# Performance work log

Measured on AMD Instinct MI355X. Metric: run time of the kernel, lower is better.

## Reference

```python
import jax, jax.numpy as jnp
import numpy as np

KERNEL_PARA = 1.0

def setup_inputs() -> dict:
    key = jax.random.key(0)
    k1, k2 = jax.random.split(key)
    H1 = jax.random.normal(k1, (8192, 64), dtype=jnp.float32)
    H2 = jax.random.normal(k2, (8192, 64), dtype=jnp.float32)
    return {"H1": H1, "H2": H2}

def reference(H1, H2):
    # S[ij] = exp(-delta * ||x_i - x_j||^2), via ||a||^2 + ||b||^2 - 2 a.b
    H11 = jnp.sum(H1 * H1, axis=1)[:, None]          # [n1, 1]
    H22 = jnp.sum(H2 * H2, axis=1)[None, :]          # [1, n2]
    H12 = jnp.matmul(H1, H2.T)                        # [n1, n2]
    D_2 = H11 + H22 - 2.0 * H12
    return jnp.exp(-KERNEL_PARA * D_2)
```

## Files before the change

kernel.cpp:

```cpp
#include <hip/hip_runtime.h>
#include <hip/hip_bf16.h>


typedef float  f32x4  __attribute__((ext_vector_type(4)));
typedef short  short8 __attribute__((ext_vector_type(8)));
typedef unsigned short ushort8 __attribute__((ext_vector_type(8)));

#define KD 64
#define TM 128
#define TN 128

__device__ __forceinline__ unsigned short f2bf(float x) {
    __hip_bfloat16 h = __float2bfloat16(x);
    unsigned short u;
    __builtin_memcpy(&u, &h, 2);
    return u;
}
__device__ __forceinline__ float bf2f(unsigned short u) {
    unsigned int v = ((unsigned int)u) << 16;
    float f;
    __builtin_memcpy(&f, &v, 4);
    return f;
}

__device__ __forceinline__ unsigned panel_off(unsigned row, unsigned kcByte) {
    return (row * 128u + kcByte) ^ ((row & 7u) << 4);
}

__global__ __launch_bounds__(512, 4) void gauss_mfma(
    const float* __restrict__ H1, const float* __restrict__ H2,
    float* __restrict__ out, int N2)
{
    __shared__ __align__(16) unsigned char sAhi[TM * KD * 2];
    __shared__ __align__(16) unsigned char sAlo[TM * KD * 2];
    __shared__ __align__(16) unsigned char sBhi[TN * KD * 2];
    __shared__ __align__(16) unsigned char sBlo[TN * KD * 2];
    __shared__ __align__(16) float snrm[TM + TN];

    const int t    = threadIdx.x;
    const int lane = t & 63, w = t >> 6;
    const int wr = w >> 2, wc = w & 3;
    const int lr = lane & 15;
    const int kb = lane >> 4;
    const int r4 = kb * 4;
    const int row0 = blockIdx.y * TM;
    const int col0 = blockIdx.x * TN;

    #pragma unroll
    for (int side = 0; side < 2; ++side) {
        const float* src = side ? (H2 + (size_t)col0 * KD)
                                : (H1 + (size_t)row0 * KD);
        unsigned char* hi = side ? sBhi : sAhi;
        unsigned char* lo = side ? sBlo : sAlo;
        #pragma unroll
        for (int i = 0; i < 2; ++i) {
            int g   = i * 512 + t;
            int row = g >> 3;
            int kc  = g & 7;
            const f32x4* p = (const f32x4*)(src + (size_t)g * 8);
            f32x4 v0 = p[0], v1 = p[1];
            ushort8 h, l;
            float s = 0.f;
            #pragma unroll
            for (int e = 0; e < 8; ++e) {
                float a = (e < 4) ? v0[e] : v1[e - 4];
                unsigned short hb = f2bf(a);
                h[e] = hb;
                l[e] = f2bf(a - bf2f(hb));
                s = fmaf(a, a, s);
            }
            s += __shfl_xor(s, 1);
            s += __shfl_xor(s, 2);
            s += __shfl_xor(s, 4);
            unsigned off = panel_off((unsigned)row, (unsigned)kc * 16u);
            *(ushort8*)(hi + off) = h;
            *(ushort8*)(lo + off) = l;
            if (kc == 0) snrm[side * TM + row] = s;
        }
    }
    __syncthreads();

    float n1v[4];
    f32x4 n2v[2];
    #pragma unroll
    for (int fr = 0; fr < 4; ++fr)
        n1v[fr] = snrm[wr * 64 + fr * 16 + lr];
    #pragma unroll
    for (int fc = 0; fc < 2; ++fc)
        n2v[fc] = *(const f32x4*)&snrm[TM + wc * 32 + fc * 16 + r4];

    f32x4 acc[4][2];
    #pragma unroll
    for (int a = 0; a < 4; ++a)
        #pragma unroll
        for (int b = 0; b < 2; ++b)
            acc[a][b] = (f32x4){0.f, 0.f, 0.f, 0.f};

    #pragma unroll
    for (int ks = 0; ks < 2; ++ks) {
        const unsigned kByte = (unsigned)(ks * 64 + kb * 16);
        short8 ah[4], al[4];
        #pragma unroll
        for (int fr = 0; fr < 4; ++fr) {
            const unsigned off = panel_off((unsigned)(wr * 64 + fr * 16 + lr), kByte);
            ah[fr] = *(const short8*)(sAhi + off);
            al[fr] = *(const short8*)(sAlo + off);
        }
        #pragma unroll
        for (int fc = 0; fc < 2; ++fc) {
            const unsigned off = panel_off((unsigned)(wc * 32 + fc * 16 + lr), kByte);
            short8 bh = *(const short8*)(sBhi + off);
            short8 bl = *(const short8*)(sBlo + off);
            #pragma unroll
            for (int fr = 0; fr < 4; ++fr) {
                acc[fr][fc] = __builtin_amdgcn_mfma_f32_16x16x32_bf16(bh, ah[fr], acc[fr][fc], 0, 0, 0);
                acc[fr][fc] = __builtin_amdgcn_mfma_f32_16x16x32_bf16(bl, ah[fr], acc[fr][fc], 0, 0, 0);
                acc[fr][fc] = __builtin_amdgcn_mfma_f32_16x16x32_bf16(bh, al[fr], acc[fr][fc], 0, 0, 0);
            }
        }
    }

    #pragma unroll
    for (int fr = 0; fr < 4; ++fr) {
        const int grow = row0 + wr * 64 + fr * 16 + lr;
        float* orow = out + (size_t)grow * (size_t)N2 + (col0 + wc * 32 + r4);
        #pragma unroll
        for (int fc = 0; fc < 2; ++fc) {
            f32x4 cst;
            #pragma unroll
            for (int j = 0; j < 4; ++j) {
                float d2 = fmaf(-2.0f, acc[fr][fc][j], n1v[fr] + n2v[fc][j]);
                cst[j] = __expf(-d2);
            }
            *(f32x4*)(orow + fc * 16) = cst;
        }
    }
}

extern "C" void kernel_launch(void* const* d_in, const int* in_sizes, int n_in,
                              void* d_out, int out_size, void* d_ws, size_t ws_size,
                              hipStream_t stream) {
    const float* H1 = (const float*)d_in[0];
    const float* H2 = (const float*)d_in[1];
    float* out = (float*)d_out;
    const int n1 = in_sizes[0] / KD;
    const int n2 = in_sizes[1] / KD;
    dim3 grid(n2 / TN, n1 / TM);
    gauss_mfma<<<grid, dim3(512), 0, stream>>>(H1, H2, out, n2);
}
```

Before: 61.90 us.

## Precompute bf16 hi/lo splits and norms in prep kernel, load fragments from global

Adds a prep kernel that splits H1 and H2 into bf16 hi/lo planes and row norms once, storing them in workspace. The main kernel then skips the per-tile conversion and the LDS staging, reading MFMA fragments straight from global memory. It uses 256-thread blocks with 4 waves, each owning a 64x64 subtile. This removes conversion work that was repeated across every tile, at the cost of an extra launch, uncoalesced-ish global fragment loads, and more accumulator registers. A fallback to the old kernel remains for when the workspace is too small.

Measured after the change: 106.8 us. 72.5% more time.

```diff
diff --git a/kernel.cpp b/kernel.cpp
--- a/kernel.cpp
+++ b/kernel.cpp
@@ -7,8 +7,11 @@
 typedef unsigned short ushort8 __attribute__((ext_vector_type(8)));
 
 #define KD 64
-#define TM 128
-#define TN 128
+
+#define PLANE  (1u << 20)
+#define OFF_N1 (4u * PLANE)
+#define OFF_N2 (4u * PLANE + 8192u * 4u)
+#define WS_NEED ((size_t)(4u * PLANE + 2u * 8192u * 4u))
 
 __device__ __forceinline__ unsigned short f2bf(float x) {
     __hip_bfloat16 h = __float2bfloat16(x);
@@ -23,40 +26,146 @@
     return f;
 }
 
+__global__ __launch_bounds__(256) void gauss_prep(const float* __restrict__ H1,
+                                                  const float* __restrict__ H2,
+                                                  unsigned char* __restrict__ ws)
+{
+    const int cid   = blockIdx.x * 256 + threadIdx.x;
+    const int which = cid >> 16;
+    const int g     = cid & 65535;
+    const int row   = g >> 3;
+    const int kc    = g & 7;
+
+    const float* src = which ? H2 : H1;
+    const f32x4* p = (const f32x4*)(src + (size_t)g * 8);
+    f32x4 v0 = p[0], v1 = p[1];
+
+    ushort8 h, l;
+    float s = 0.f;
+    #pragma unroll
+    for (int e = 0; e < 8; ++e) {
+        float a = (e < 4) ? v0[e] : v1[e - 4];
+        unsigned short hb = f2bf(a);
+        h[e] = hb;
+        l[e] = f2bf(a - bf2f(hb));
+        s = fmaf(a, a, s);
+    }
+    s += __shfl_xor(s, 1);
+    s += __shfl_xor(s, 2);
+    s += __shfl_xor(s, 4);
+
+    unsigned char* hi = ws + (which ? 2u * PLANE : 0u) + (size_t)g * 16u;
+    unsigned char* lo = hi + PLANE;
+    *(ushort8*)hi = h;
+    *(ushort8*)lo = l;
+    if (kc == 0)
+        *(float*)(ws + (which ? OFF_N2 : OFF_N1) + (size_t)row * 4u) = s;
+}
+
+__global__ __launch_bounds__(256, 3) void gauss_main(
+    const unsigned char* __restrict__ ws, float* __restrict__ out, int N2)
+{
+    const int t    = threadIdx.x;
+    const int lane = t & 63, w = t >> 6;
+    const int wr = w >> 1, wc = w & 1;
+    const int lr = lane & 15;
+    const int kb = lane >> 4;
+    const int r4 = kb * 4;
+    const int row0 = blockIdx.y * 128;
+    const int col0 = blockIdx.x * 128;
+
+    const unsigned char* hi1 = ws;
+    const unsigned char* lo1 = ws + PLANE;
+    const unsigned char* hi2 = ws + 2u * PLANE;
+    const unsigned char* lo2 = ws + 3u * PLANE;
+    const float* nrm1 = (const float*)(ws + OFF_N1);
+    const float* nrm2 = (const float*)(ws + OFF_N2);
+
+    float n1v[4];
+    f32x4 n2v[4];
+    #pragma unroll
+    for (int fr = 0; fr < 4; ++fr)
+        n1v[fr] = nrm1[row0 + wr * 64 + fr * 16 + lr];
+    #pragma unroll
+    for (int fc = 0; fc < 4; ++fc)
+        n2v[fc] = *(const f32x4*)(nrm2 + col0 + wc * 64 + fc * 16 + r4);
+
+    f32x4 acc[4][4];
+    #pragma unroll
+    for (int a = 0; a < 4; ++a)
+        #pragma unroll
+        for (int b = 0; b < 4; ++b)
+            acc[a][b] = (f32x4){0.f, 0.f, 0.f, 0.f};
+
+    #pragma unroll
+    for (int ks = 0; ks < 2; ++ks) {
+        const unsigned kByte = (unsigned)(ks * 64 + kb * 16);
+        short8 ah[4], al[4];
+        #pragma unroll
+        for (int fr = 0; fr < 4; ++fr) {
+            size_t off = (size_t)(row0 + wr * 64 + fr * 16 + lr) * 128u + kByte;
+            ah[fr] = *(const short8*)(hi1 + off);
+            al[fr] = *(const short8*)(lo1 + off);
+        }
+        #pragma unroll
+        for (int fc = 0; fc < 4; ++fc) {
+            size_t off = (size_t)(col0 + wc * 64 + fc * 16 + lr) * 128u + kByte;
+            short8 bh = *(const short8*)(hi2 + off);
+            short8 bl = *(const short8*)(lo2 + off);
+            #pragma unroll
+            for (int fr = 0; fr < 4; ++fr) {
+                acc[fr][fc] = __builtin_amdgcn_mfma_f32_16x16x32_bf16(bh, ah[fr], acc[fr][fc], 0, 0, 0);
+                acc[fr][fc] = __builtin_amdgcn_mfma_f32_16x16x32_bf16(bl, ah[fr], acc[fr][fc], 0, 0, 0);
+                acc[fr][fc] = __builtin_amdgcn_mfma_f32_16x16x32_bf16(bh, al[fr], acc[fr][fc], 0, 0, 0);
+            }
+        }
+    }
+
+    #pragma unroll
+    for (int fr = 0; fr < 4; ++fr) {
+        const int grow = row0 + wr * 64 + fr * 16 + lr;
+        float* orow = out + (size_t)grow * (size_t)N2 + (col0 + wc * 64 + r4);
+        #pragma unroll
+        for (int fc = 0; fc < 4; ++fc) {
+            f32x4 cst;
+            #pragma unroll
+            for (int j = 0; j < 4; ++j) {
+                float d2 = fmaf(-2.0f, acc[fr][fc][j], n1v[fr] + n2v[fc][j]);
+                cst[j] = __expf(-d2);
+            }
+            *(f32x4*)(orow + fc * 16) = cst;
+        }
+    }
+}
+
 __device__ __forceinline__ unsigned panel_off(unsigned row, unsigned kcByte) {
     return (row * 128u + kcByte) ^ ((row & 7u) << 4);
 }
 
-__global__ __launch_bounds__(512, 4) void gauss_mfma(
+__global__ __launch_bounds__(512, 4) void gauss_fallback(
     const float* __restrict__ H1, const float* __restrict__ H2,
     float* __restrict__ out, int N2)
 {
-    __shared__ __align__(16) unsigned char sAhi[TM * KD * 2];
-    __shared__ __align__(16) unsigned char sAlo[TM * KD * 2];
-    __shared__ __align__(16) unsigned char sBhi[TN * KD * 2];
-    __shared__ __align__(16) unsigned char sBlo[TN * KD * 2];
-    __shared__ __align__(16) float snrm[TM + TN];
+    __shared__ __align__(16) unsigned char sAhi[128 * 128];
+    __shared__ __align__(16) unsigned char sAlo[128 * 128];
+    __shared__ __align__(16) unsigned char sBhi[128 * 128];
+    __shared__ __align__(16) unsigned char sBlo[128 * 128];
+    __shared__ __align__(16) float snrm[256];
 
     const int t    = threadIdx.x;
     const int lane = t & 63, w = t >> 6;
     const int wr = w >> 2, wc = w & 3;
-    const int lr = lane & 15;
-    const int kb = lane >> 4;
-    const int r4 = kb * 4;
-    const int row0 = blockIdx.y * TM;
-    const int col0 = blockIdx.x * TN;
+    const int lr = lane & 15, kb = lane >> 4, r4 = kb * 4;
+    const int row0 = blockIdx.y * 128, col0 = blockIdx.x * 128;
 
     #pragma unroll
     for (int side = 0; side < 2; ++side) {
-        const float* src = side ? (H2 + (size_t)col0 * KD)
-                                : (H1 + (size_t)row0 * KD);
+        const float* src = side ? (H2 + (size_t)col0 * KD) : (H1 + (size_t)row0 * KD);
         unsigned char* hi = side ? sBhi : sAhi;
         unsigned char* lo = side ? sBlo : sAlo;
         #pragma unroll
         for (int i = 0; i < 2; ++i) {
-            int g   = i * 512 + t;
-            int row = g >> 3;
-            int kc  = g & 7;
+            int g = i * 512 + t, row = g >> 3, kc = g & 7;
             const f32x4* p = (const f32x4*)(src + (size_t)g * 8);
             f32x4 v0 = p[0], v1 = p[1];
             ushort8 h, l;
@@ -75,7 +184,7 @@
             unsigned off = panel_off((unsigned)row, (unsigned)kc * 16u);
             *(ushort8*)(hi + off) = h;
             *(ushort8*)(lo + off) = l;
-            if (kc == 0) snrm[side * TM + row] = s;
+            if (kc == 0) snrm[side * 128 + row] = s;
         }
     }
     __syncthreads();
@@ -83,11 +192,9 @@
     float n1v[4];
     f32x4 n2v[2];
     #pragma unroll
-    for (int fr = 0; fr < 4; ++fr)
-        n1v[fr] = snrm[wr * 64 + fr * 16 + lr];
-    #pragma unroll
-    for (int fc = 0; fc < 2; ++fc)
-        n2v[fc] = *(const f32x4*)&snrm[TM + wc * 32 + fc * 16 + r4];
+    for (int fr = 0; fr < 4; ++fr) n1v[fr] = snrm[wr * 64 + fr * 16 + lr];
+    #pragma unroll
+    for (int fc = 0; fc < 2; ++fc) n2v[fc] = *(const f32x4*)&snrm[128 + wc * 32 + fc * 16 + r4];
 
     f32x4 acc[4][2];
     #pragma unroll
@@ -145,6 +252,12 @@
     float* out = (float*)d_out;
     const int n1 = in_sizes[0] / KD;
     const int n2 = in_sizes[1] / KD;
-    dim3 grid(n2 / TN, n1 / TM);
-    gauss_mfma<<<grid, dim3(512), 0, stream>>>(H1, H2, out, n2);
-}
+    dim3 grid(n2 / 128, n1 / 128);
+
+    if (ws_size >= WS_NEED) {
+        gauss_prep<<<dim3(512), dim3(256), 0, stream>>>(H1, H2, (unsigned char*)d_ws);
+        gauss_main<<<grid, dim3(256), 0, stream>>>((const unsigned char*)d_ws, out, n2);
+    } else {
+        gauss_fallback<<<grid, dim3(512), 0, stream>>>(H1, H2, out, n2);
+    }
+}
```
